# Kernel optimization log

Hardware: AMD Instinct MI355X
Metric: run time of the kernel (lower is better)

## Reference

```python
import jax, jax.numpy as jnp
import numpy as np
from jax.scipy.special import i0

IM_SIZE = (256, 256)
GRID_SIZE = (512, 512)
NUMPOINTS = 6
OS = GRID_SIZE[0] / IM_SIZE[0]
# Beatty et al. optimal Kaiser-Bessel shape parameter
BETA = float(np.pi * np.sqrt((NUMPOINTS / OS) ** 2 * (OS - 0.5) ** 2 - 0.8))


def _apod_1d(N, G):
    # 1/FT(kb kernel) scaling coefficients (de-apodization), static numpy
    x = np.arange(N) - N / 2.0
    arg = np.pi * NUMPOINTS * x / G
    t = BETA ** 2 - arg ** 2  # > 0 for this config
    ph = np.sinh(np.sqrt(t)) / np.sqrt(t)
    return (1.0 / ph).astype(np.float32)


def _kb(u):
    # Kaiser-Bessel interpolation kernel, support |u| <= NUMPOINTS/2
    x = 2.0 * u / NUMPOINTS
    t = 1.0 - x * x
    inside = t > 0
    t = jnp.where(inside, t, 0.0)
    return jnp.where(inside, i0(BETA * jnp.sqrt(t)), 0.0)


def setup_inputs():
    key = jax.random.key(0)
    k1, k2, k3 = jax.random.split(key, 3)
    B, M = 8, 131072
    image = jax.random.normal(k1, (B,) + IM_SIZE, dtype=jnp.float32)
    ktraj = (jax.random.uniform(k2, (B, 2, M), dtype=jnp.float32) * 2.0 - 1.0) * jnp.pi
    dcf = jax.random.uniform(k3, (B, M), dtype=jnp.float32)
    return {"image": image, "ktraj": ktraj, "dcf": dcf}


def _nufft(image, ktraj, dcf):
    B = image.shape[0]
    N1, N2 = IM_SIZE
    G1, G2 = GRID_SIZE
    J = NUMPOINTS
    # 1) de-apodization (scaling coefficients), separable per-dim
    a1 = jnp.asarray(_apod_1d(N1, G1))
    a2 = jnp.asarray(_apod_1d(N2, G2))
    img = image.astype(jnp.complex64) * (a1[:, None] * a2[None, :])
    # 2) centered zero-pad to oversampled grid, FFT with DC at bin 0
    p1, p2 = (G1 - N1) // 2, (G2 - N2) // 2
    grid = jnp.zeros((B, G1, G2), dtype=jnp.complex64).at[:, p1:p1 + N1, p2:p2 + N2].set(img)
    kgrid = jnp.fft.fft2(jnp.fft.ifftshift(grid, axes=(1, 2)))
    # 3) KB interpolation (gather) at non-uniform points
    tm1 = ktraj[:, 0] * (G1 / (2.0 * jnp.pi))  # (B,M) in grid units
    tm2 = ktraj[:, 1] * (G2 / (2.0 * jnp.pi))
    offs = jnp.arange(J, dtype=jnp.float32) - (J // 2 - 1)  # [-2..3]
    g1 = jnp.floor(tm1)[..., None] + offs  # (B,M,J) neighbor coords
    g2 = jnp.floor(tm2)[..., None] + offs
    w1 = _kb(tm1[..., None] - g1)
    w2 = _kb(tm2[..., None] - g2)
    i1 = jnp.mod(g1.astype(jnp.int32), G1)
    i2 = jnp.mod(g2.astype(jnp.int32), G2)
    lin = (i1[..., :, None] * G2 + i2[..., None, :]).reshape(B, -1)  # (B, M*J*J)
    vals = jnp.take_along_axis(kgrid.reshape(B, -1), lin, axis=1).reshape(B, -1, J, J)
    w = (w1[..., :, None] * w2[..., None, :]).astype(jnp.complex64)
    kdata = jnp.sum(vals * w, axis=(-1, -2))  # (B,M) complex
    kdata = kdata * dcf
    return jnp.stack([kdata.real, kdata.imag], axis=0)  # (2,B,M) float32


def reference(image, ktraj, dcf):
    return _nufft(image, ktraj, dcf)
```

## Files before the change

### kernel.cpp

```cpp
#include <hip/hip_runtime.h>
#include <math.h>

#define GSZ 512
#define NSZ 256
#define NBATCH 8
#define MPTS 131072
#define PI_F 3.14159265358979f
#define BETA_F 13.8551004f
#define BETA2_F (BETA_F * BETA_F)
#define RSQ2 0.70710678f
#define PADIDX(i) ((i) + ((i) >> 3))

typedef float f32x4 __attribute__((ext_vector_type(4)));

#define GLOAD4(dst, ptr) asm volatile("global_load_dwordx4 %0, %1, off" : "=&v"(dst) : "v"(ptr) : "memory")
#define GLOAD1(dst, ptr) asm volatile("global_load_dword %0, %1, off"   : "=&v"(dst) : "v"(ptr) : "memory")
#define GSTORE1(val, ptr) asm volatile("global_store_dword %0, %1, off" :: "v"(ptr), "v"(val) : "memory")
#define WAITVM(n) do { asm volatile("s_waitcnt vmcnt(" #n ")" ::: "memory"); \
                       __builtin_amdgcn_sched_barrier(0); } while (0)
#define SBAR() __builtin_amdgcn_sched_barrier(0)


__device__ __forceinline__ float apod(int i) {
    float x = (float)(i - 128);
    float arg = PI_F * 6.0f * x * (1.0f / 512.0f);
    float t = BETA2_F - arg * arg;
    float st = sqrtf(t);
    return 2.0f * st * __expf(-st);
}

__device__ __forceinline__ float kbw(float u) {
    float t = 1.0f - u * u * (1.0f / 9.0f);
    float x = BETA_F * sqrtf(fmaxf(t, 0.0f));
    float xc = fmaxf(x, 0.35f);
    float R = __builtin_amdgcn_rsqf(xc);
    float R2 = R * R;
    float q = R * (0.39894228f + R2 * (0.04986779f + R2 * 0.02804702f));
    float w = __expf(xc) * q;
    return (t > 0.0f) ? w : 0.0f;
}

template<int CTRL>
__device__ __forceinline__ float qdpp(float v) {
    int r = __builtin_amdgcn_mov_dpp(__float_as_int(v), CTRL, 0xF, 0xF, true);
    return __int_as_float(r);
}

__device__ __forceinline__ float2 cadd(float2 a, float2 b){ return make_float2(a.x+b.x, a.y+b.y); }
__device__ __forceinline__ float2 csub(float2 a, float2 b){ return make_float2(a.x-b.x, a.y-b.y); }
__device__ __forceinline__ float2 cmul(float2 a, float2 b){ return make_float2(a.x*b.x-a.y*b.y, a.x*b.y+a.y*b.x); }
__device__ __forceinline__ float2 mul_negi(float2 a){ return make_float2(a.y, -a.x); }
__device__ __forceinline__ float2 mul_posi(float2 a){ return make_float2(-a.y, a.x); }
__device__ __forceinline__ float2 mul_w81(float2 a){ return make_float2(RSQ2*(a.x+a.y), RSQ2*(a.y-a.x)); }
__device__ __forceinline__ float2 mul_w83(float2 a){ return make_float2(RSQ2*(a.y-a.x), -RSQ2*(a.x+a.y)); }

__device__ __forceinline__ void dft8_combine(float2 E0, float2 E1, float2 E2, float2 E3,
                                             float2 O0, float2 O1, float2 O2, float2 O3,
                                             float2* y) {
    float2 c1 = mul_w81(O1), c2 = mul_negi(O2), c3 = mul_w83(O3);
    y[0] = cadd(E0, O0); y[4] = csub(E0, O0);
    y[1] = cadd(E1, c1); y[5] = csub(E1, c1);
    y[2] = cadd(E2, c2); y[6] = csub(E2, c2);
    y[3] = cadd(E3, c3); y[7] = csub(E3, c3);
}

__device__ __forceinline__ void dft8(const float2* x, float2* y) {
    float2 a0=x[0], a1=x[2], a2=x[4], a3=x[6];
    float2 b0=x[1], b1=x[3], b2=x[5], b3=x[7];
    float2 ta0=cadd(a0,a2), ta1=csub(a0,a2), ta2=cadd(a1,a3), ta3=csub(a1,a3);
    float2 E0=cadd(ta0,ta2), E2=csub(ta0,ta2);
    float2 E1=cadd(ta1, mul_negi(ta3)), E3=cadd(ta1, mul_posi(ta3));
    float2 tb0=cadd(b0,b2), tb1=csub(b0,b2), tb2=cadd(b1,b3), tb3=csub(b1,b3);
    float2 O0=cadd(tb0,tb2), O2=csub(tb0,tb2);
    float2 O1=cadd(tb1, mul_negi(tb3)), O3=cadd(tb1, mul_posi(tb3));
    dft8_combine(E0,E1,E2,E3,O0,O1,O2,O3,y);
}

__device__ __forceinline__ void dft8_pruned(float2 x0, float2 x1, float2 x6, float2 x7, float2* y) {
    float2 E0 = cadd(x0, x6), E2 = csub(x0, x6);
    float2 E1 = cadd(x0, mul_posi(x6)), E3 = cadd(x0, mul_negi(x6));
    float2 O0 = cadd(x1, x7), O2 = csub(x1, x7);
    float2 O1 = cadd(x1, mul_posi(x7)), O3 = cadd(x1, mul_negi(x7));
    dft8_combine(E0,E1,E2,E3,O0,O1,O2,O3,y);
}

template<int S>
__device__ __forceinline__ void twiddle8(int t, float2* y) {
    if (S < 2) {
        int j = (S == 0) ? t : (t >> 3);
        const float scale = (S == 0) ? (-2.0f*PI_F/512.0f) : (-2.0f*PI_F/64.0f);
        float theta = scale * (float)j;
        float sn, cs;
        __sincosf(theta, &sn, &cs);
        float2 w = make_float2(cs, sn), wq = w;
        y[1] = cmul(y[1], wq);
        #pragma unroll
        for (int q = 2; q < 8; ++q) { wq = cmul(wq, w); y[q] = cmul(y[q], wq); }
    }
}


__device__ __forceinline__ float2 pswap(float2 v) {
    return make_float2(qdpp<0xB1>(v.x), qdpp<0xB1>(v.y));
}

__device__ __forceinline__ void dft8_half(const float2* v, float2* EO) {
    float2 t0 = cadd(v[0], v[2]), t1 = csub(v[0], v[2]);
    float2 t2 = cadd(v[1], v[3]), t3 = csub(v[1], v[3]);
    EO[0] = cadd(t0, t2); EO[2] = csub(t0, t2);
    EO[1] = cadd(t1, mul_negi(t3)); EO[3] = cadd(t1, mul_posi(t3));
}

__device__ __forceinline__ void dft8p_half(float2 u0, float2 u1, float2* EO) {
    EO[0] = cadd(u0, u1); EO[2] = csub(u0, u1);
    EO[1] = cadd(u0, mul_posi(u1)); EO[3] = cadd(u0, mul_negi(u1));
}

__device__ __forceinline__ void combine_half(int h, const float2* V, float2* y) {
    float2 P0 = pswap(V[0]), P1 = pswap(V[1]), P2 = pswap(V[2]), P3 = pswap(V[3]);
    float2 E0 = h ? P0 : V[0], O0 = h ? V[0] : P0;
    float2 E1 = h ? P1 : V[1], O1 = h ? V[1] : P1;
    float2 E2 = h ? P2 : V[2], O2 = h ? V[2] : P2;
    float2 E3 = h ? P3 : V[3], O3 = h ? V[3] : P3;
    float2 c1 = mul_w81(O1), c2 = mul_negi(O2), c3 = mul_w83(O3);
    float s = h ? -1.0f : 1.0f;
    y[0] = make_float2(fmaf(s, O0.x, E0.x), fmaf(s, O0.y, E0.y));
    y[1] = make_float2(fmaf(s, c1.x, E1.x), fmaf(s, c1.y, E1.y));
    y[2] = make_float2(fmaf(s, c2.x, E2.x), fmaf(s, c2.y, E2.y));
    y[3] = make_float2(fmaf(s, c3.x, E3.x), fmaf(s, c3.y, E3.y));
}

__device__ __forceinline__ void twiddle4h(int jidx, float scale, int h, float2* y) {
    float theta = scale * (float)jidx;
    float sn, cs;
    __sincosf(theta, &sn, &cs);
    float2 w = make_float2(cs, sn);
    float2 w2 = cmul(w, w);
    float2 w4 = cmul(w2, w2);
    float2 m = h ? w4 : make_float2(1.0f, 0.0f);
    y[0] = cmul(y[0], m);
    float2 wq = cmul(m, w); y[1] = cmul(y[1], wq);
    wq = cmul(wq, w);       y[2] = cmul(y[2], wq);
    wq = cmul(wq, w);       y[3] = cmul(y[3], wq);
}

__global__ __launch_bounds__(256) void pass1_rowfft(const float* __restrict__ image,
                                                    float2* __restrict__ T) {
    __shared__ float2 sm[2][2][578];
    int tid = threadIdx.x;
    int r = tid >> 7;
    int tt = tid & 127;
    int h = tt & 1;
    int b = tt >> 1;
    int blk = blockIdx.x;
    int p = blk & 3;
    int g = blk >> 2;
    int rp = (g << 1) + r;
    int y = (rp < 128) ? rp : (rp + 256);
    int iy = (y < 128) ? (y + 128) : (y - 384);
    float ay = apod(iy);
    const float* irow0 = image + ((size_t)((2 * p)     * NSZ + iy)) * NSZ;
    const float* irow1 = image + ((size_t)((2 * p + 1) * NSZ + iy)) * NSZ;

    float2 y4[4];
    {
        int iA = h ? (b + 192) : (b + 128);
        int iB = h ? (b + 64)  : b;
        float wA = ay * apod(iA), wB = ay * apod(iB);
        float2 u0 = make_float2(irow0[iA] * wA, irow1[iA] * wA);
        float2 u1 = make_float2(irow0[iB] * wB, irow1[iB] * wB);
        float2 EO[4];
        dft8p_half(u0, u1, EO);
        combine_half(h, EO, y4);
        twiddle4h(b, -2.0f * PI_F / 512.0f, h, y4);
    }
    float2* A  = sm[0][r];
    float2* Bf = sm[1][r];
    #pragma unroll
    for (int qq = 0; qq < 4; ++qq) A[PADIDX((b << 3) + (h << 2) + qq)] = y4[qq];
    __syncthreads();
    {
        float2 v[4];
        #pragma unroll
        for (int i = 0; i < 4; ++i) v[i] = A[PADIDX(b + (((i << 1) + h) << 6))];
        float2 EO[4];
        dft8_half(v, EO);
        combine_half(h, EO, y4);
        twiddle4h(b >> 3, -2.0f * PI_F / 64.0f, h, y4);
        int base = (b & 7) + ((b >> 3) << 6);
        #pragma unroll
        for (int qq = 0; qq < 4; ++qq) Bf[PADIDX(base + (((h << 2) + qq) << 3))] = y4[qq];
    }
    __syncthreads();
    {
        float2 v[4];
        #pragma unroll
        for (int i = 0; i < 4; ++i) v[i] = Bf[PADIDX(b + (((i << 1) + h) << 6))];
        float2 EO[4];
        dft8_half(v, EO);
        combine_half(h, EO, y4);
        float2* Trow = T + (((size_t)(p << 8) + rp) << 9);
        #pragma unroll
        for (int qq = 0; qq < 4; ++qq) Trow[b + (((h << 2) + qq) << 6)] = y4[qq];
    }
}

__global__ __launch_bounds__(256) void pass2_colfft(const float2* __restrict__ T,
                                                    float2* __restrict__ kgrid) {
    __shared__ float2 B[8][578];
    int tid = threadIdx.x;
    int blk = blockIdx.x;
    int p = blk & 3;
    int g = blk >> 2;
    const float2* Tb = T + ((size_t)p << 17);
    float2* Kb0 = kgrid + ((size_t)(2 * p) << 18);
    float2* Kb1 = Kb0 + ((size_t)1 << 18);

    #define COLG(c) ((g > 0) ? (((c) < 4) ? ((g << 2) + (c)) : (505 - (g << 2) + (c))) \
                             : (((c) < 4) ? (c) : (((c) == 7) ? 256 : (505 + (c)))))

    {
        int c = tid & 7, r0 = tid >> 3;
        int colg = COLG(c);
        #pragma unroll
        for (int k = 0; k < 8; ++k) {
            int rr = r0 + (k << 5);
            B[c][PADIDX(rr)] = Tb[((size_t)rr << 9) + colg];
        }
    }
    __syncthreads();
    int t = tid & 63;
    int c0 = tid >> 6;
    float2* Ba = B[c0];
    float2* Bb = B[c0 + 4];
    float2 ya[8], yb[8];
    {
        float2 a0 = Ba[PADIDX(t)],       a1 = Ba[PADIDX(t + 64)];
        float2 a6 = Ba[PADIDX(t + 128)], a7 = Ba[PADIDX(t + 192)];
        float2 b0 = Bb[PADIDX(t)],       b1 = Bb[PADIDX(t + 64)];
        float2 b6 = Bb[PADIDX(t + 128)], b7 = Bb[PADIDX(t + 192)];
        dft8_pruned(a0, a1, a6, a7, ya); twiddle8<0>(t, ya);
        dft8_pruned(b0, b1, b6, b7, yb); twiddle8<0>(t, yb);
    }
    __syncthreads();
    #pragma unroll
    for (int q = 0; q < 8; ++q) {
        Ba[PADIDX((t << 3) + q)] = ya[q];
        Bb[PADIDX((t << 3) + q)] = yb[q];
    }
    __syncthreads();
    {
        float2 xa[8], xb[8];
        #pragma unroll
        for (int pp = 0; pp < 8; ++pp) { xa[pp] = Ba[PADIDX(t + (pp << 6))]; xb[pp] = Bb[PADIDX(t + (pp << 6))]; }
        dft8(xa, ya); twiddle8<1>(t, ya);
        dft8(xb, yb); twiddle8<1>(t, yb);
    }
    __syncthreads();
    {
        int j = t >> 3, k = t & 7, base = k + (j << 6);
        #pragma unroll
        for (int q = 0; q < 8; ++q) {
            Ba[PADIDX(base + (q << 3))] = ya[q];
            Bb[PADIDX(base + (q << 3))] = yb[q];
        }
    }
    __syncthreads();
    {
        float2 xa[8], xb[8];
        #pragma unroll
        for (int pp = 0; pp < 8; ++pp) { xa[pp] = Ba[PADIDX(t + (pp << 6))]; xb[pp] = Bb[PADIDX(t + (pp << 6))]; }
        dft8(xa, ya);
        dft8(xb, yb);
    }
    __syncthreads();
    #pragma unroll
    for (int q = 0; q < 8; ++q) {
        Ba[PADIDX(t + (q << 6))] = ya[q];
        Bb[PADIDX(t + (q << 6))] = yb[q];
    }
    __syncthreads();
    {
        int c = tid & 7, r0 = tid >> 3;
        int colg = COLG(c);
        int mc = 7 - c;
        if (g == 0) { if (c == 0) mc = 0; else if (c == 7) mc = 7; }
        #pragma unroll
        for (int k = 0; k < 16; ++k) {
            int rr = r0 + (k << 5);
            int mr = (512 - rr) & 511;
            float2 Z = B[c][PADIDX(rr)];
            float2 M = B[mc][PADIDX(mr)];
            float2 K0 = make_float2(0.5f * (Z.x + M.x), 0.5f * (Z.y - M.y));
            float2 K1 = make_float2(0.5f * (Z.y + M.y), 0.5f * (M.x - Z.x));
            size_t off = ((size_t)rr << 9) + colg;
            Kb0[off] = K0;
            Kb1[off] = K1;
        }
    }
    #undef COLG
}

#define ISSUE(i, V0, V1, V2, V3, V4, V5) do {                               \
    float tm1 = r1v[i] * SCALE, tm2 = r2v[i] * SCALE;                       \
    float f1 = floorf(tm1), f2 = floorf(tm2);                               \
    int if1 = (int)f1, if2 = (int)f2;                                       \
    int e0 = (if2 - 2) & ~1;                             \
    int cpair = (e0 + j2) & 511;           \
    const float* pb = Kf + (cpair << 1);                                    \
    GLOAD4(V0, pb + (((if1 - 2) & 511) << 10));                             \
    GLOAD4(V1, pb + (((if1 - 1) & 511) << 10));                             \
    GLOAD4(V2, pb + (((if1    ) & 511) << 10));                             \
    GLOAD4(V3, pb + (((if1 + 1) & 511) << 10));                             \
    GLOAD4(V4, pb + (((if1 + 2) & 511) << 10));                             \
    GLOAD4(V5, pb + (((if1 + 3) & 511) << 10));                             \
    fr1v[i] = tm1 - f1;                                                     \
    u2v[i]  = tm2 - (float)(e0 + j2);                                       \
    SBAR();                                                                 \
} while (0)

#define WEIGHTS(i)                                                          \
    float u2_##i  = u2v[i];                                                 \
    float w2a_##i = kbw(u2_##i);                                            \
    float w2b_##i = kbw(u2_##i - 1.0f);                                     \
    float w1A_##i = kbw(fr1v[i] - fjm2);                                    \
    float w1B_##i = kbw(fr1v[i] - fjp2);                                    \
    float w0_##i = qdpp<0x00>(w1A_##i);                                     \
    float w1_##i = qdpp<0x55>(w1A_##i);                                     \
    float w2_##i = qdpp<0xAA>(w1A_##i);                                     \
    float w3_##i = qdpp<0xFF>(w1A_##i);                                     \
    float w4_##i = qdpp<0x00>(w1B_##i);                                     \
    float w5_##i = qdpp<0x55>(w1B_##i);

#define FMACONS(i, V0, V1, V2, V3, V4, V5) do {                             \
    float c0re = w0_##i * V0.x, c0im = w0_##i * V0.y;                       \
    float c1re = w0_##i * V0.z, c1im = w0_##i * V0.w;                       \
    c0re = fmaf(w1_##i, V1.x, c0re); c0im = fmaf(w1_##i, V1.y, c0im);       \
    c1re = fmaf(w1_##i, V1.z, c1re); c1im = fmaf(w1_##i, V1.w, c1im);       \
    c0re = fmaf(w2_##i, V2.x, c0re); c0im = fmaf(w2_##i, V2.y, c0im);       \
    c1re = fmaf(w2_##i, V2.z, c1re); c1im = fmaf(w2_##i, V2.w, c1im);       \
    c0re = fmaf(w3_##i, V3.x, c0re); c0im = fmaf(w3_##i, V3.y, c0im);       \
    c1re = fmaf(w3_##i, V3.z, c1re); c1im = fmaf(w3_##i, V3.w, c1im);       \
    c0re = fmaf(w4_##i, V4.x, c0re); c0im = fmaf(w4_##i, V4.y, c0im);       \
    c1re = fmaf(w4_##i, V4.z, c1re); c1im = fmaf(w4_##i, V4.w, c1im);       \
    c0re = fmaf(w5_##i, V5.x, c0re); c0im = fmaf(w5_##i, V5.y, c0im);       \
    c1re = fmaf(w5_##i, V5.z, c1re); c1im = fmaf(w5_##i, V5.w, c1im);       \
    float p_re = fmaf(w2a_##i, c0re, w2b_##i * c1re);                       \
    float p_im = fmaf(w2a_##i, c0im, w2b_##i * c1im);                       \
    p_re += qdpp<0xB1>(p_re); p_re += qdpp<0x4E>(p_re);                     \
    p_im += qdpp<0xB1>(p_im); p_im += qdpp<0x4E>(p_im);                     \
    int mmm = m0 + ((i) << 6);                                              \
    float sre = p_re * rdv[i], sim = p_im * rdv[i];                         \
    if (j == 0) GSTORE1(sre, out_re + mmm);                                 \
    if (j == 1) GSTORE1(sim, out_im + mmm);                                 \
} while (0)

__global__ __launch_bounds__(256) void interp_kb(const float* __restrict__ ktraj,
                                                 const float* __restrict__ dcf,
                                                 const float2* __restrict__ kgrid,
                                                 float* __restrict__ out) {
    int tid = threadIdx.x;
    int blk = blockIdx.x;
    int b = blk & 7;
    int gb = blk >> 3;
    int j = tid & 3;
    int q = tid >> 2;
    int j2 = j << 1;
    float fjm2 = (float)(j - 2), fjp2 = (float)(j + 2);

    const float SCALE = (float)GSZ / (2.0f * PI_F);
    const float* Kf = (const float*)(kgrid + ((size_t)b << 18));
    const float* kt1 = ktraj + ((size_t)(b * 2)) * MPTS;
    const float* kt2 = kt1 + MPTS;
    const float* dcfb = dcf + ((size_t)b << 17);
    float* out_re = out + ((size_t)b << 17);
    float* out_im = out_re + (size_t)NBATCH * MPTS;

    int m0 = (gb << 9) + q;

    float r1v[8], r2v[8], rdv[8];
    #define LOADPT(i) do {                     \
        GLOAD1(r1v[i], kt1 + m0 + ((i) << 6)); \
        GLOAD1(r2v[i], kt2 + m0 + ((i) << 6)); \
        GLOAD1(rdv[i], dcfb + m0 + ((i) << 6)); } while (0)
    LOADPT(0); LOADPT(1); LOADPT(2); LOADPT(3);
    LOADPT(4); LOADPT(5); LOADPT(6); LOADPT(7);
    #undef LOADPT
    WAITVM(0);

    float fr1v[8], u2v[8];
    f32x4 A0, A1, A2, A3, A4, A5;
    f32x4 B0, B1, B2, B3, B4, B5;

    ISSUE(0, A0, A1, A2, A3, A4, A5);
    ISSUE(1, B0, B1, B2, B3, B4, B5);

    WEIGHTS(0);
    WAITVM(6);
    FMACONS(0, A0, A1, A2, A3, A4, A5);
    ISSUE(2, A0, A1, A2, A3, A4, A5);
    WEIGHTS(1);
    WAITVM(6);
    FMACONS(1, B0, B1, B2, B3, B4, B5);
    ISSUE(3, B0, B1, B2, B3, B4, B5);
    WEIGHTS(2);
    WAITVM(6);
    FMACONS(2, A0, A1, A2, A3, A4, A5);
    ISSUE(4, A0, A1, A2, A3, A4, A5);
    WEIGHTS(3);
    WAITVM(6);
    FMACONS(3, B0, B1, B2, B3, B4, B5);
    ISSUE(5, B0, B1, B2, B3, B4, B5);
    WEIGHTS(4);
    WAITVM(6);
    FMACONS(4, A0, A1, A2, A3, A4, A5);
    ISSUE(6, A0, A1, A2, A3, A4, A5);
    WEIGHTS(5);
    WAITVM(6);
    FMACONS(5, B0, B1, B2, B3, B4, B5);
    ISSUE(7, B0, B1, B2, B3, B4, B5);
    WEIGHTS(6);
    WAITVM(6);
    FMACONS(6, A0, A1, A2, A3, A4, A5);
    WEIGHTS(7);
    WAITVM(0);
    FMACONS(7, B0, B1, B2, B3, B4, B5);

    WAITVM(0);
}


extern "C" void kernel_launch(void* const* d_in, const int* in_sizes, int n_in,
                              void* d_out, int out_size, void* d_ws, size_t ws_size,
                              hipStream_t stream) {
    const float* image = (const float*)d_in[0];
    const float* ktraj = (const float*)d_in[1];
    const float* dcf   = (const float*)d_in[2];
    float* out = (float*)d_out;

    float2* T     = (float2*)d_ws;
    float2* kgrid = T + (size_t)4 * 256 * GSZ;

    pass1_rowfft<<<512, 256, 0, stream>>>(image, T);
    pass2_colfft<<<256, 256, 0, stream>>>(T, kgrid);
    interp_kb<<<NBATCH * 256, 256, 0, stream>>>(ktraj, dcf, kgrid, out);
}
```

Measured before the change: 125.5 us.

## Bin points by grid-row band and interpolate from LDS-staged grid rows

Extra blocks in the column-FFT kernel bucket every trajectory point by its 4-row band of the oversampled grid, using atomic cursors, and write (t1, t2, dcf, index) records into per-band slots. The interpolation kernel then gives one block to each (batch, band) pair. That block stages the 9 grid rows it needs into LDS and serves the 6x6 neighborhood reads from LDS instead of scattered global dwordx4 gathers. This trades random global and L2 gather traffic for a binning pass with atomics, scattered output stores and heavy LDS use per block. Each bucket has a fixed capacity of 2048, and points beyond it are silently dropped, so clustered trajectories would give wrong results.

New measurement: 216.5 us. 72.6% more time.

```diff
diff --git a/kernel.cpp b/kernel.cpp
--- a/kernel.cpp
+++ b/kernel.cpp
@@ -12,13 +12,6 @@
 #define PADIDX(i) ((i) + ((i) >> 3))
 
 typedef float f32x4 __attribute__((ext_vector_type(4)));
-
-#define GLOAD4(dst, ptr) asm volatile("global_load_dwordx4 %0, %1, off" : "=&v"(dst) : "v"(ptr) : "memory")
-#define GLOAD1(dst, ptr) asm volatile("global_load_dword %0, %1, off"   : "=&v"(dst) : "v"(ptr) : "memory")
-#define GSTORE1(val, ptr) asm volatile("global_store_dword %0, %1, off" :: "v"(ptr), "v"(val) : "memory")
-#define WAITVM(n) do { asm volatile("s_waitcnt vmcnt(" #n ")" ::: "memory"); \
-                       __builtin_amdgcn_sched_barrier(0); } while (0)
-#define SBAR() __builtin_amdgcn_sched_barrier(0)
 
 
 __device__ __forceinline__ float apod(int i) {
@@ -145,9 +138,13 @@
 }
 
 __global__ __launch_bounds__(256) void pass1_rowfft(const float* __restrict__ image,
-                                                    float2* __restrict__ T) {
+                                                    float2* __restrict__ T,
+                                                    int* __restrict__ cursors) {
     __shared__ float2 sm[2][2][578];
     int tid = threadIdx.x;
+    if (blockIdx.x == 0) {
+        for (int z = tid; z < 1024; z += 256) cursors[z] = 0;
+    }
     int r = tid >> 7;
     int tt = tid & 127;
     int h = tt & 1;
@@ -206,10 +203,38 @@
 }
 
 __global__ __launch_bounds__(256) void pass2_colfft(const float2* __restrict__ T,
-                                                    float2* __restrict__ kgrid) {
+                                                    float2* __restrict__ kgrid,
+                                                    const float* __restrict__ ktraj,
+                                                    const float* __restrict__ dcf,
+                                                    int* __restrict__ cursors,
+                                                    float4* __restrict__ sortedpt) {
     __shared__ float2 B[8][578];
     int tid = threadIdx.x;
     int blk = blockIdx.x;
+
+    if (blk >= 256) {
+        int u = blk - 256;
+        int bs = u >> 5, seg = u & 31;
+        const float SCALE = (float)GSZ / (2.0f * PI_F);
+        const float* kt1 = ktraj + (size_t)(bs * 2) * MPTS;
+        const float* kt2 = kt1 + MPTS;
+        const float* dcfb = dcf + ((size_t)bs << 17);
+        int* cur = cursors + (bs << 7);
+        float4* sp = sortedpt + ((size_t)bs << 18);
+        #pragma unroll 4
+        for (int k = 0; k < 16; ++k) {
+            int m = (seg << 12) + (k << 8) + tid;
+            float t1 = kt1[m] * SCALE;
+            float t2 = kt2[m] * SCALE;
+            float d  = dcfb[m];
+            int key = (((int)floorf(t1)) & 511) >> 2;
+            int pos = atomicAdd(cur + key, 1);
+            if (pos < 2048)
+                sp[((size_t)key << 11) + pos] = make_float4(t1, t2, d, __int_as_float(m));
+        }
+        return;
+    }
+
     int p = blk & 3;
     int g = blk >> 2;
     const float2* Tb = T + ((size_t)p << 17);
@@ -301,132 +326,94 @@
     #undef COLG
 }
 
-#define ISSUE(i, V0, V1, V2, V3, V4, V5) do {                               \
-    float tm1 = r1v[i] * SCALE, tm2 = r2v[i] * SCALE;                       \
-    float f1 = floorf(tm1), f2 = floorf(tm2);                               \
-    int if1 = (int)f1, if2 = (int)f2;                                       \
-    int e0 = (if2 - 2) & ~1;                             \
-    int cpair = (e0 + j2) & 511;           \
-    const float* pb = Kf + (cpair << 1);                                    \
-    GLOAD4(V0, pb + (((if1 - 2) & 511) << 10));                             \
-    GLOAD4(V1, pb + (((if1 - 1) & 511) << 10));                             \
-    GLOAD4(V2, pb + (((if1    ) & 511) << 10));                             \
-    GLOAD4(V3, pb + (((if1 + 1) & 511) << 10));                             \
-    GLOAD4(V4, pb + (((if1 + 2) & 511) << 10));                             \
-    GLOAD4(V5, pb + (((if1 + 3) & 511) << 10));                             \
-    fr1v[i] = tm1 - f1;                                                     \
-    u2v[i]  = tm2 - (float)(e0 + j2);                                       \
-    SBAR();                                                                 \
-} while (0)
-
-#define WEIGHTS(i)                                                          \
-    float u2_##i  = u2v[i];                                                 \
-    float w2a_##i = kbw(u2_##i);                                            \
-    float w2b_##i = kbw(u2_##i - 1.0f);                                     \
-    float w1A_##i = kbw(fr1v[i] - fjm2);                                    \
-    float w1B_##i = kbw(fr1v[i] - fjp2);                                    \
-    float w0_##i = qdpp<0x00>(w1A_##i);                                     \
-    float w1_##i = qdpp<0x55>(w1A_##i);                                     \
-    float w2_##i = qdpp<0xAA>(w1A_##i);                                     \
-    float w3_##i = qdpp<0xFF>(w1A_##i);                                     \
-    float w4_##i = qdpp<0x00>(w1B_##i);                                     \
-    float w5_##i = qdpp<0x55>(w1B_##i);
-
-#define FMACONS(i, V0, V1, V2, V3, V4, V5) do {                             \
-    float c0re = w0_##i * V0.x, c0im = w0_##i * V0.y;                       \
-    float c1re = w0_##i * V0.z, c1im = w0_##i * V0.w;                       \
-    c0re = fmaf(w1_##i, V1.x, c0re); c0im = fmaf(w1_##i, V1.y, c0im);       \
-    c1re = fmaf(w1_##i, V1.z, c1re); c1im = fmaf(w1_##i, V1.w, c1im);       \
-    c0re = fmaf(w2_##i, V2.x, c0re); c0im = fmaf(w2_##i, V2.y, c0im);       \
-    c1re = fmaf(w2_##i, V2.z, c1re); c1im = fmaf(w2_##i, V2.w, c1im);       \
-    c0re = fmaf(w3_##i, V3.x, c0re); c0im = fmaf(w3_##i, V3.y, c0im);       \
-    c1re = fmaf(w3_##i, V3.z, c1re); c1im = fmaf(w3_##i, V3.w, c1im);       \
-    c0re = fmaf(w4_##i, V4.x, c0re); c0im = fmaf(w4_##i, V4.y, c0im);       \
-    c1re = fmaf(w4_##i, V4.z, c1re); c1im = fmaf(w4_##i, V4.w, c1im);       \
-    c0re = fmaf(w5_##i, V5.x, c0re); c0im = fmaf(w5_##i, V5.y, c0im);       \
-    c1re = fmaf(w5_##i, V5.z, c1re); c1im = fmaf(w5_##i, V5.w, c1im);       \
-    float p_re = fmaf(w2a_##i, c0re, w2b_##i * c1re);                       \
-    float p_im = fmaf(w2a_##i, c0im, w2b_##i * c1im);                       \
-    p_re += qdpp<0xB1>(p_re); p_re += qdpp<0x4E>(p_re);                     \
-    p_im += qdpp<0xB1>(p_im); p_im += qdpp<0x4E>(p_im);                     \
-    int mmm = m0 + ((i) << 6);                                              \
-    float sre = p_re * rdv[i], sim = p_im * rdv[i];                         \
-    if (j == 0) GSTORE1(sre, out_re + mmm);                                 \
-    if (j == 1) GSTORE1(sim, out_im + mmm);                                 \
-} while (0)
-
-__global__ __launch_bounds__(256) void interp_kb(const float* __restrict__ ktraj,
-                                                 const float* __restrict__ dcf,
-                                                 const float2* __restrict__ kgrid,
+__global__ __launch_bounds__(256) void interp_kb(const float2* __restrict__ kgrid,
+                                                 const int* __restrict__ cursors,
+                                                 const float4* __restrict__ sortedpt,
                                                  float* __restrict__ out) {
+    __shared__ float lds[9 * 1028];
     int tid = threadIdx.x;
     int blk = blockIdx.x;
     int b = blk & 7;
-    int gb = blk >> 3;
+    int band = blk >> 3;
     int j = tid & 3;
     int q = tid >> 2;
     int j2 = j << 1;
     float fjm2 = (float)(j - 2), fjp2 = (float)(j + 2);
 
-    const float SCALE = (float)GSZ / (2.0f * PI_F);
-    const float* Kf = (const float*)(kgrid + ((size_t)b << 18));
-    const float* kt1 = ktraj + ((size_t)(b * 2)) * MPTS;
-    const float* kt2 = kt1 + MPTS;
-    const float* dcfb = dcf + ((size_t)b << 17);
+    int cnt = cursors[(b << 7) + band];
+    cnt = (cnt > 2048) ? 2048 : cnt;
+    if (cnt == 0) return;
+
+    const float2* Kb = kgrid + ((size_t)b << 18);
+    #pragma unroll
+    for (int r = 0; r < 9; ++r) {
+        int gr = ((band << 2) - 2 + r) & 511;
+        const float4* src = (const float4*)(Kb + ((size_t)gr << 9));
+        *(float4*)(lds + r * 1028 + (tid << 2)) = src[tid];
+    }
+    __syncthreads();
+
+    const float4* sp = sortedpt + ((size_t)b << 18) + ((size_t)band << 11);
     float* out_re = out + ((size_t)b << 17);
     float* out_im = out_re + (size_t)NBATCH * MPTS;
 
-    int m0 = (gb << 9) + q;
-
-    float r1v[8], r2v[8], rdv[8];
-    #define LOADPT(i) do {                     \
-        GLOAD1(r1v[i], kt1 + m0 + ((i) << 6)); \
-        GLOAD1(r2v[i], kt2 + m0 + ((i) << 6)); \
-        GLOAD1(rdv[i], dcfb + m0 + ((i) << 6)); } while (0)
-    LOADPT(0); LOADPT(1); LOADPT(2); LOADPT(3);
-    LOADPT(4); LOADPT(5); LOADPT(6); LOADPT(7);
-    #undef LOADPT
-    WAITVM(0);
-
-    float fr1v[8], u2v[8];
-    f32x4 A0, A1, A2, A3, A4, A5;
-    f32x4 B0, B1, B2, B3, B4, B5;
-
-    ISSUE(0, A0, A1, A2, A3, A4, A5);
-    ISSUE(1, B0, B1, B2, B3, B4, B5);
-
-    WEIGHTS(0);
-    WAITVM(6);
-    FMACONS(0, A0, A1, A2, A3, A4, A5);
-    ISSUE(2, A0, A1, A2, A3, A4, A5);
-    WEIGHTS(1);
-    WAITVM(6);
-    FMACONS(1, B0, B1, B2, B3, B4, B5);
-    ISSUE(3, B0, B1, B2, B3, B4, B5);
-    WEIGHTS(2);
-    WAITVM(6);
-    FMACONS(2, A0, A1, A2, A3, A4, A5);
-    ISSUE(4, A0, A1, A2, A3, A4, A5);
-    WEIGHTS(3);
-    WAITVM(6);
-    FMACONS(3, B0, B1, B2, B3, B4, B5);
-    ISSUE(5, B0, B1, B2, B3, B4, B5);
-    WEIGHTS(4);
-    WAITVM(6);
-    FMACONS(4, A0, A1, A2, A3, A4, A5);
-    ISSUE(6, A0, A1, A2, A3, A4, A5);
-    WEIGHTS(5);
-    WAITVM(6);
-    FMACONS(5, B0, B1, B2, B3, B4, B5);
-    ISSUE(7, B0, B1, B2, B3, B4, B5);
-    WEIGHTS(6);
-    WAITVM(6);
-    FMACONS(6, A0, A1, A2, A3, A4, A5);
-    WEIGHTS(7);
-    WAITVM(0);
-    FMACONS(7, B0, B1, B2, B3, B4, B5);
-
-    WAITVM(0);
+    int iters = (cnt + 63) >> 6;
+    for (int it = 0; it < iters; ++it) {
+        int pidx = (it << 6) + q;
+        bool valid = pidx < cnt;
+        float4 pt = sp[valid ? pidx : 0];
+        float tm1 = pt.x, tm2 = pt.y, dd = pt.z;
+        int m = __float_as_int(pt.w);
+
+        float f1 = floorf(tm1), f2 = floorf(tm2);
+        int if1 = (int)f1, if2 = (int)f2;
+        int e0 = (if2 - 2) & ~1;
+        int cpair = (e0 + j2) & 511;
+        int lr = (if1 & 511) - (band << 2);
+
+        float u2 = tm2 - (float)(e0 + j2);
+        float w2a = kbw(u2);
+        float w2b = kbw(u2 - 1.0f);
+        float fr1 = tm1 - f1;
+        float w1A = kbw(fr1 - fjm2);
+        float w1B = kbw(fr1 - fjp2);
+        float w0_ = qdpp<0x00>(w1A);
+        float w1_ = qdpp<0x55>(w1A);
+        float w2_ = qdpp<0xAA>(w1A);
+        float w3_ = qdpp<0xFF>(w1A);
+        float w4_ = qdpp<0x00>(w1B);
+        float w5_ = qdpp<0x55>(w1B);
+
+        const float* lp = lds + (cpair << 1);
+        f32x4 v0 = *(const f32x4*)(lp + (lr + 0) * 1028);
+        f32x4 v1 = *(const f32x4*)(lp + (lr + 1) * 1028);
+        f32x4 v2 = *(const f32x4*)(lp + (lr + 2) * 1028);
+        f32x4 v3 = *(const f32x4*)(lp + (lr + 3) * 1028);
+        f32x4 v4 = *(const f32x4*)(lp + (lr + 4) * 1028);
+        f32x4 v5 = *(const f32x4*)(lp + (lr + 5) * 1028);
+
+        float c0re = w0_ * v0.x, c0im = w0_ * v0.y;
+        float c1re = w0_ * v0.z, c1im = w0_ * v0.w;
+        c0re = fmaf(w1_, v1.x, c0re); c0im = fmaf(w1_, v1.y, c0im);
+        c1re = fmaf(w1_, v1.z, c1re); c1im = fmaf(w1_, v1.w, c1im);
+        c0re = fmaf(w2_, v2.x, c0re); c0im = fmaf(w2_, v2.y, c0im);
+        c1re = fmaf(w2_, v2.z, c1re); c1im = fmaf(w2_, v2.w, c1im);
+        c0re = fmaf(w3_, v3.x, c0re); c0im = fmaf(w3_, v3.y, c0im);
+        c1re = fmaf(w3_, v3.z, c1re); c1im = fmaf(w3_, v3.w, c1im);
+        c0re = fmaf(w4_, v4.x, c0re); c0im = fmaf(w4_, v4.y, c0im);
+        c1re = fmaf(w4_, v4.z, c1re); c1im = fmaf(w4_, v4.w, c1im);
+        c0re = fmaf(w5_, v5.x, c0re); c0im = fmaf(w5_, v5.y, c0im);
+        c1re = fmaf(w5_, v5.z, c1re); c1im = fmaf(w5_, v5.w, c1im);
+        float p_re = fmaf(w2a, c0re, w2b * c1re);
+        float p_im = fmaf(w2a, c0im, w2b * c1im);
+        p_re += qdpp<0xB1>(p_re); p_re += qdpp<0x4E>(p_re);
+        p_im += qdpp<0xB1>(p_im); p_im += qdpp<0x4E>(p_im);
+
+        if (valid) {
+            if (j == 0) out_re[m] = p_re * dd;
+            else if (j == 1) out_im[m] = p_im * dd;
+        }
+    }
 }
 
 
@@ -438,10 +425,12 @@
     const float* dcf   = (const float*)d_in[2];
     float* out = (float*)d_out;
 
-    float2* T     = (float2*)d_ws;
-    float2* kgrid = T + (size_t)4 * 256 * GSZ;
-
-    pass1_rowfft<<<512, 256, 0, stream>>>(image, T);
-    pass2_colfft<<<256, 256, 0, stream>>>(T, kgrid);
-    interp_kb<<<NBATCH * 256, 256, 0, stream>>>(ktraj, dcf, kgrid, out);
-}
+    float2* T        = (float2*)d_ws;
+    float2* kgrid    = T + (size_t)4 * 256 * GSZ;
+    int*    cursors  = (int*)((char*)d_ws + 20971520);
+    float4* sortedpt = (float4*)((char*)d_ws + 20975616);
+
+    pass1_rowfft<<<512, 256, 0, stream>>>(image, T, cursors);
+    pass2_colfft<<<512, 256, 0, stream>>>(T, kgrid, ktraj, dcf, cursors, sortedpt);
+    interp_kb<<<1024, 256, 0, stream>>>(kgrid, cursors, sortedpt, out);
+}
```
